# Kernel optimization log

Hardware: AMD Instinct MI355X
Metric: run time of the kernel (lower is better)

The kernel has to match this reference:

```python
import jax, jax.numpy as jnp
import numpy as np
from jax import lax

# Static model/config sizes
B, ANG, C, H, NF, NB = 1, 9, 3, 128, 16, 2


def get_freq_position(n):
    """Anti-diagonal frequency bands of an n x n angular-DCT grid (python/static)."""
    bands = []
    for i in range(n):
        bands.append(([i], [0]))
    for j in range(1, n):
        bands.append(([n - 1], [j]))
    for item in bands:
        while item[0][0] > 0 and item[1][0] < n - 1:
            item[0].insert(0, item[0][0] - 1)
            item[1].insert(0, item[1][0] + 1)
    return bands


def dct_mat(n):
    """Orthonormal DCT-II matrix (row k = k-th basis)."""
    k = jnp.arange(n, dtype=jnp.float32)[:, None]
    i = jnp.arange(n, dtype=jnp.float32)[None, :]
    m = jnp.cos(jnp.pi * (i + 0.5) * k / n) * jnp.sqrt(2.0 / n)
    return m.at[0].multiply(1.0 / np.sqrt(2.0))


def conv3d(x, w, b):
    # x: (N, Cin, D, H, W), w: (Cout, Cin, 3, 3, 3)
    y = lax.conv_general_dilated(x, w, (1, 1, 1), 'SAME',
                                 dimension_numbers=('NCDHW', 'OIDHW', 'NCDHW'))
    return y + b[None, :, None, None, None]


def branch(cut, wi, bi, a, wb, bb):
    """init conv + NB ResBlock3D (PReLU -> Conv3d, residual), plus outer skip."""
    y0 = conv3d(cut, wi, bi)
    y = y0
    for k in range(NB):
        r = jnp.where(y >= 0, y, a[k] * y)  # PReLU (single-parameter)
        y = y + conv3d(r, wb[k], bb[k])
    return y0 + y


def setup_inputs() -> dict:
    key = jax.random.key(0)
    ks = jax.random.split(key, 32)

    def nrm(k, shape, s=0.05):
        return jax.random.normal(k, shape, dtype=jnp.float32) * s

    inp = {"x": jax.random.normal(ks[0], (B, ANG, ANG, C, H, H), dtype=jnp.float32)}
    i = 1
    for n in ("dc", "lo", "mi", "hi"):
        inp[f"w_{n}_i"] = nrm(ks[i], (NF, C, 3, 3, 3)); i += 1
        inp[f"b_{n}_i"] = nrm(ks[i], (NF,)); i += 1
        inp[f"a_{n}"] = jnp.full((NB,), 0.25, dtype=jnp.float32)
        inp[f"w_{n}"] = nrm(ks[i], (NB, NF, NF, 3, 3, 3)); i += 1
        inp[f"b_{n}"] = nrm(ks[i], (NB, NF)); i += 1
    inp["w_last"] = nrm(ks[i], (C, NF))  # 1x1 Conv2d, no bias
    return inp


def reference(x, w_dc_i, b_dc_i, a_dc, w_dc, b_dc,
              w_lo_i, b_lo_i, a_lo, w_lo, b_lo,
              w_mi_i, b_mi_i, a_mi, w_mi, b_mi,
              w_hi_i, b_hi_i, a_hi, w_hi, b_hi, w_last):
    b, u, v, c, h, w = x.shape
    Da = dct_mat(u)  # angular DCT (u == v)
    Ds = dct_mat(h)  # spatial DCT (h == w)

    # SpaAngDCT: spatial 2D DCT then angular 2D DCT
    xf = jnp.einsum('buvchw,Hh,Ww->buvcHW', x, Ds, Ds)
    xf = jnp.einsum('buvchw,Uu,Vv->bUVchw', xf, Da, Da)

    x_rec = jnp.zeros((b, NF, u, v, h, w), dtype=x.dtype)
    for idx, (ui, vi) in enumerate(get_freq_position(u)):
        if idx == 0:
            p = (w_dc_i, b_dc_i, a_dc, w_dc, b_dc)
        elif idx <= 2:
            p = (w_lo_i, b_lo_i, a_lo, w_lo, b_lo)
        elif idx <= u - 1:
            p = (w_mi_i, b_mi_i, a_mi, w_mi, b_mi)
        else:
            p = (w_hi_i, b_hi_i, a_hi, w_hi, b_hi)
        ua, va = jnp.array(ui), jnp.array(vi)
        cut = xf[:, ua, va].transpose(0, 2, 1, 3, 4)  # (b, c, L, h, w)
        out = branch(cut, *p)                          # (b, NF, L, h, w)
        x_rec = x_rec.at[:, :, ua, va].set(out)        # scatter band back

    # 'b c u v h w -> b c (u h) (v w)' then 1x1 conv (NF -> 3)
    xr = x_rec.transpose(0, 1, 2, 4, 3, 5).reshape(b, NF, u * h, v * w)
    xr = jnp.einsum('bnHW,on->boHW', xr, w_last)
    xr = xr.reshape(b, c, u, h, v, w).transpose(0, 2, 4, 1, 3, 5)  # (b,u,v,c,h,w)

    # InverseSpaAngDCT: angular IDCT then spatial IDCT
    xr = jnp.einsum('bUVchw,Uu,Vv->buvchw', xr, Da, Da)
    xr = jnp.einsum('buvcHW,Hh,Ww->buvchw', xr, Ds, Ds)
    return xr + x
```

## Files before the change

kernel.cpp:

```cpp
#include <hip/hip_runtime.h>
#include <hip/hip_bf16.h>
#include <math.h>

typedef __hip_bfloat16 bf16;
typedef __attribute__((ext_vector_type(8))) short short8;
typedef __attribute__((ext_vector_type(4))) float floatx4;
typedef __attribute__((ext_vector_type(4))) unsigned int uint4v;
typedef __attribute__((ext_vector_type(2))) unsigned int uint2v;

#define HW 16384
#define NSLICE 243

__constant__ int c_s_of_p[81] = {
  0, 1,1, 2,2,2, 3,3,3,3, 4,4,4,4,4, 5,5,5,5,5,5, 6,6,6,6,6,6,6,
  7,7,7,7,7,7,7,7, 8,8,8,8,8,8,8,8,8, 9,9,9,9,9,9,9,9,
  10,10,10,10,10,10,10, 11,11,11,11,11,11, 12,12,12,12,12,
  13,13,13,13, 14,14,14, 15,15, 16};
__constant__ int c_l_of_p[81] = {
  0, 0,1, 0,1,2, 0,1,2,3, 0,1,2,3,4, 0,1,2,3,4,5, 0,1,2,3,4,5,6,
  0,1,2,3,4,5,6,7, 0,1,2,3,4,5,6,7,8, 0,1,2,3,4,5,6,7,
  0,1,2,3,4,5,6, 0,1,2,3,4,5, 0,1,2,3,4, 0,1,2,3, 0,1,2, 0,1, 0};
__constant__ int c_L_of_s[17] = {1,2,3,4,5,6,7,8,9,8,7,6,5,4,3,2,1};
__constant__ int c_g_of_s[17] = {0,1,1,2,2,2,2,2,2,3,3,3,3,3,3,3,3};
__constant__ int c_pos_uv[81] = {
  0,1,3,6,10,15,21,28,36,
  2,4,7,11,16,22,29,37,45,
  5,8,12,17,23,30,38,46,53,
  9,13,18,24,31,39,47,54,60,
  14,19,25,32,40,48,55,61,66,
  20,26,33,41,49,56,62,67,71,
  27,34,42,50,57,63,68,72,75,
  35,43,51,58,64,69,73,76,78,
  44,52,59,65,70,74,77,79,80};

struct WPtrs {
  const float* wi[4]; const float* bi[4]; const float* a[4];
  const float* wb[4]; const float* bb[4]; const float* wl;
};

__device__ __forceinline__ unsigned short f2bf(float f) {
  return __bfloat16_as_ushort(__float2bfloat16(f));
}
__device__ __forceinline__ float bf2f(unsigned short u) {
  return __uint_as_float(((unsigned int)u) << 16);
}
__device__ __forceinline__ float bflo(unsigned int w) {
  return __uint_as_float(w << 16);
}
__device__ __forceinline__ float bfhi(unsigned int w) {
  return __uint_as_float(w & 0xffff0000u);
}
__device__ __forceinline__ unsigned int pack2(float a, float b) {
  return (unsigned int)f2bf(a) | ((unsigned int)f2bf(b) << 16);
}
__device__ __forceinline__ float invprelu(float v, float invA) {
  return (v >= 0.f) ? v : v * invA;
}
__device__ __forceinline__ void bfsplit(float v, unsigned short& hi, unsigned short& lo) {
  unsigned int bits = __float_as_uint(v);
  hi = (unsigned short)(bits >> 16);
  lo = f2bf(v - __uint_as_float(bits & 0xffff0000u));
}
__device__ __forceinline__ void gl_lds16(const void* g, void* l) {
  __builtin_amdgcn_global_load_lds(
      (const __attribute__((address_space(1))) unsigned int*)g,
      (__attribute__((address_space(3))) unsigned int*)l, 16, 0, 0);
}
__device__ __forceinline__ int ldsoff(int plane, int col) {
  return plane * 2112 + ((plane & 3) << 5) + (col << 4);
}
__device__ __forceinline__ float da_entry(int t) {
  int U = t / 9, u = t % 9;
  if (U == 0) return 0.33333334f;
  int m9 = (U * (2 * u + 1)) % 36;
  return cosf((float)m9 * 0.17453293f) * 0.47140452f;
}
__device__ __forceinline__ void wmf_repack(const WPtrs& P, unsigned short* Wmf, int t) {
  if (t >= 92160) return;
  int s = t / 7680, r = t % 7680;
  int step = r / 512, r2 = r % 512;
  int lane = r2 >> 3, j = r2 & 7;
  int d = step / 5, i = step % 5;
  int q = lane >> 4, m = lane & 15;
  int tl = 2 * i + (q >> 1);
  int cin = (q & 1) * 8 + j;
  float val = 0.f;
  if (tl <= 8) {
    int ky = tl / 3, kx = tl % 3;
    int tap = d * 9 + ky * 3 + kx;
    if (s < 4) {
      if (cin < 3) val = P.wi[s][(m * 3 + cin) * 27 + tap];
    } else {
      int g = (s - 4) >> 1, k = (s - 4) & 1;
      val = P.wb[g][((k * 16 + m) * 16 + cin) * 27 + tap];
    }
  }
  Wmf[t] = f2bf(val);
}

__global__ __launch_bounds__(1024) void k_dct2(const float* __restrict__ X,
                                               const float* __restrict__ xres,
                                               float* __restrict__ Yf,
                                               unsigned short* __restrict__ Ybf,
                                               WPtrs P,
                                               unsigned short* __restrict__ Wmf) {
  if (blockIdx.x >= 243) {
    int t2 = (blockIdx.x - 243) * 1024 + threadIdx.x;
    wmf_repack(P, Wmf, t2);
    return;
  }
  extern __shared__ char dynlds[];
  unsigned short* sThi = (unsigned short*)dynlds;
  unsigned short* sTlo = (unsigned short*)(dynlds + 34816);
  unsigned short* sBhi = (unsigned short*)(dynlds + 69632);
  unsigned short* sBlo = (unsigned short*)(dynlds + 102400);
  int s = blockIdx.x;
  int t = threadIdx.x;
  int lane = t & 63, wv16 = t >> 6;
  int mt8 = wv16 & 7, nh = wv16 >> 3;
  int q = lane >> 4, n16 = lane & 15;
  const float* Xs = X + (size_t)s * HW;
  int isFwd = (Ybf != nullptr);

  for (int i = t; i < 16384; i += 1024) {
    int jj = i & 7, ln = (i >> 3) & 63, ks = (i >> 9) & 3, tile = i >> 11;
    int row = tile * 16 + (ln & 15);
    int colk = ks * 32 + (ln >> 4) * 8 + jj;
    int mm = isFwd ? (row * (2 * colk + 1)) & 511
                   : (colk * (2 * row + 1)) & 511;
    float vv = cosf((float)mm * 0.012271846f) * 0.125f;
    if (isFwd ? (row == 0) : (colk == 0)) vv *= 0.70710678f;
    unsigned short hh, ll;
    bfsplit(vv, hh, ll);
    sBhi[i] = hh; sBlo[i] = ll;
  }
  __syncthreads();

  floatx4 acc[4];
#pragma unroll
  for (int ntl = 0; ntl < 4; ntl++) acc[ntl] = (floatx4){0.f, 0.f, 0.f, 0.f};

#pragma unroll
  for (int ks = 0; ks < 4; ks++) {
    short8 ahi, alo;
    {
      const float* xp = Xs + (mt8 * 16 + n16) * 128 + ks * 32 + q * 8;
      float4 a = *(const float4*)xp;
      float4 b = *(const float4*)(xp + 4);
      union { short8 v; unsigned short u[8]; } H, L;
      float xv[8] = {a.x, a.y, a.z, a.w, b.x, b.y, b.z, b.w};
#pragma unroll
      for (int j = 0; j < 8; j++) bfsplit(xv[j], H.u[j], L.u[j]);
      ahi = H.v; alo = L.v;
    }
#pragma unroll
    for (int ntl = 0; ntl < 4; ntl++) {
      int e = (nh * 4 + ntl) * 2048 + ks * 512 + lane * 8;
      short8 bh = *(const short8*)(sBhi + e);
      short8 bl = *(const short8*)(sBlo + e);
      acc[ntl] = __builtin_amdgcn_mfma_f32_16x16x32_bf16(ahi, bl, acc[ntl], 0, 0, 0);
      acc[ntl] = __builtin_amdgcn_mfma_f32_16x16x32_bf16(alo, bh, acc[ntl], 0, 0, 0);
      acc[ntl] = __builtin_amdgcn_mfma_f32_16x16x32_bf16(ahi, bh, acc[ntl], 0, 0, 0);
    }
  }

#pragma unroll
  for (int ntl = 0; ntl < 4; ntl++) {
    int col = (nh * 4 + ntl) * 16 + n16;
    int rowb = mt8 * 16 + q * 4;
#pragma unroll
    for (int rp = 0; rp < 4; rp += 2) {
      unsigned short h0, l0, h1, l1;
      bfsplit(acc[ntl][rp], h0, l0);
      bfsplit(acc[ntl][rp + 1], h1, l1);
      int widx = (col * 136 + rowb + rp) >> 1;
      ((unsigned int*)sThi)[widx] = (unsigned int)h0 | ((unsigned int)h1 << 16);
      ((unsigned int*)sTlo)[widx] = (unsigned int)l0 | ((unsigned int)l1 << 16);
    }
  }
  __syncthreads();

#pragma unroll
  for (int ntl = 0; ntl < 4; ntl++) acc[ntl] = (floatx4){0.f, 0.f, 0.f, 0.f};

#pragma unroll
  for (int ks = 0; ks < 4; ks++) {
    int e0 = mt8 * 2048 + ks * 512 + lane * 8;
    short8 ahi = *(const short8*)(sBhi + e0);
    short8 alo = *(const short8*)(sBlo + e0);
#pragma unroll
    for (int ntl = 0; ntl < 4; ntl++) {
      int off = ((nh * 4 + ntl) * 16 + n16) * 136 + ks * 32 + q * 8;
      short8 bh = *(const short8*)(sThi + off);
      short8 bl = *(const short8*)(sTlo + off);
      acc[ntl] = __builtin_amdgcn_mfma_f32_16x16x32_bf16(ahi, bl, acc[ntl], 0, 0, 0);
      acc[ntl] = __builtin_amdgcn_mfma_f32_16x16x32_bf16(alo, bh, acc[ntl], 0, 0, 0);
      acc[ntl] = __builtin_amdgcn_mfma_f32_16x16x32_bf16(ahi, bh, acc[ntl], 0, 0, 0);
    }
  }

#pragma unroll
  for (int ntl = 0; ntl < 4; ntl++) {
    int row0 = mt8 * 16 + q * 4;
    int col = (nh * 4 + ntl) * 16 + n16;
#pragma unroll
    for (int r = 0; r < 4; r++) {
      size_t oi = (size_t)s * HW + (size_t)(row0 + r) * 128 + col;
      float v = acc[ntl][r];
      if (Ybf) {
        Ybf[oi] = f2bf(v);
      } else {
        if (xres) v += xres[oi];
        Yf[oi] = v;
      }
    }
  }
}

__global__ __launch_bounds__(256) void k_angfwd(const unsigned short* __restrict__ in,
                                                unsigned short* __restrict__ out) {
  __shared__ float sDa[81];
  int t = threadIdx.x;
  if (t < 81) sDa[t] = da_entry(t);
  __syncthreads();
  int idx = blockIdx.x * 256 + t;
  int hw = idx & (HW - 1);
  int r = idx >> 14;
  int c = r % 3, ub = r / 3;
  unsigned short raw[81];
#pragma unroll
  for (int u = 0; u < 9; u++)
#pragma unroll
    for (int v = 0; v < 9; v++)
      raw[u * 9 + v] = in[(size_t)((u * 9 + v) * 3 + c) * HW + hw];
  float tmp[3][9];
#pragma unroll
  for (int i = 0; i < 3; i++)
#pragma unroll
    for (int v = 0; v < 9; v++) tmp[i][v] = 0.f;
#pragma unroll
  for (int u = 0; u < 9; u++) {
    float fv[9];
#pragma unroll
    for (int v = 0; v < 9; v++) fv[v] = bf2f(raw[u * 9 + v]);
#pragma unroll
    for (int i = 0; i < 3; i++) {
      float dc = sDa[(ub * 3 + i) * 9 + u];
#pragma unroll
      for (int v = 0; v < 9; v++) tmp[i][v] += dc * fv[v];
    }
  }
#pragma unroll
  for (int i = 0; i < 3; i++) {
    int U = ub * 3 + i;
#pragma unroll
    for (int V = 0; V < 9; V++) {
      float acc = 0.f;
#pragma unroll
      for (int v = 0; v < 9; v++) acc += sDa[V * 9 + v] * tmp[i][v];
      out[(size_t)(c_pos_uv[U * 9 + V] * 3 + c) * HW + hw] = f2bf(acc);
    }
  }
}

__global__ __launch_bounds__(256) void k_anginv(const float* __restrict__ xrb,
                                                float* __restrict__ out) {
  __shared__ float sDa[81];
  int t = threadIdx.x;
  if (t < 81) sDa[t] = da_entry(t);
  __syncthreads();
  int idx = blockIdx.x * 256 + t;
  int hw = idx & (HW - 1);
  int r = idx >> 14;
  int c = r % 3, ub = r / 3;
  float raw[81];
#pragma unroll
  for (int U = 0; U < 9; U++)
#pragma unroll
    for (int V = 0; V < 9; V++)
      raw[U * 9 + V] = xrb[((size_t)c_pos_uv[U * 9 + V] * 3 + c) * HW + hw];
  float tmp[3][9];
#pragma unroll
  for (int i = 0; i < 3; i++)
#pragma unroll
    for (int V = 0; V < 9; V++) tmp[i][V] = 0.f;
#pragma unroll
  for (int U = 0; U < 9; U++) {
#pragma unroll
    for (int i = 0; i < 3; i++) {
      float dc = sDa[U * 9 + (ub * 3 + i)];
#pragma unroll
      for (int V = 0; V < 9; V++) tmp[i][V] += dc * raw[U * 9 + V];
    }
  }
#pragma unroll
  for (int i = 0; i < 3; i++) {
    int u = ub * 3 + i;
#pragma unroll
    for (int v = 0; v < 9; v++) {
      float acc = 0.f;
#pragma unroll
      for (int V = 0; V < 9; V++) acc += sDa[V * 9 + v] * tmp[i][V];
      out[(size_t)((u * 9 + v) * 3 + c) * HW + hw] = acc;
    }
  }
}

__global__ __launch_bounds__(1024, 8) void k_conv(const unsigned short* __restrict__ src,
                                              const unsigned short* __restrict__ act0,
                                              const unsigned short* __restrict__ Wmf,
                                              WPtrs P,
                                              int sel,
                                              unsigned short* __restrict__ boutAct,
                                              float* __restrict__ xrbOut) {
  __shared__ unsigned short s_lds[21184];
  int p = blockIdx.y;
  int s = c_s_of_p[p], l = c_l_of_p[p];
  int g = c_g_of_s[s], Ls = c_L_of_s[s];
  int row0 = blockIdx.x * 8;
  int t = threadIdx.x;
  int lane = t & 63, wv16 = t >> 6;
  int row8 = wv16 & 7, ch = wv16 >> 3;
  int q = lane >> 4, n = lane & 15;

  float aNext = (sel < 2) ? P.a[g][sel] : 0.f;
  float invA  = (sel > 0) ? 1.0f / P.a[g][sel - 1] : 0.f;

  {
    uint4v z = (uint4v){0u, 0u, 0u, 0u};
    int zmax = (sel == 0) ? 1320 : 40;
    for (int i = t; i < zmax; i += 1024) {
      int row, half, col;
      if (i < 40) { row = i >> 2; half = (i >> 1) & 1; col = (i & 1) ? 129 : 0; }
      else { int j = i - 40; row = j >> 7; col = (j & 127) + 1; half = 1; }
      *(uint4v*)((char*)s_lds + ldsoff(row * 2 + half, col)) = z;
    }
    for (int row = 0; row < 10; row++) {
      int grow = row0 - 1 + row;
      if ((unsigned)grow >= 128u) {
        for (int i = t; i < 264; i += 1024) {
          int half = i / 132, col = i % 132;
          *(uint4v*)((char*)s_lds + ldsoff(row * 2 + half, col)) = z;
        }
      }
    }
  }

  int off2[5];
#pragma unroll
  for (int i = 0; i < 5; i++) {
    int tl = 2 * i + (q >> 1);
    if (tl > 8) tl = 8;
    int ky = tl / 3, kx = tl % 3;
    off2[i] = ldsoff(2 * (row8 + ky) + (q & 1), n + kx) + ch * 1024;
  }

  int setIdx = (sel == 0) ? g : (4 + g * 2 + (sel - 1));
  const char* WsetBase = (const char*)Wmf + (size_t)setIdx * 15 * 1024;

  floatx4 acc[4];
#pragma unroll
  for (int cg = 0; cg < 4; cg++) acc[cg] = (floatx4){0.f, 0.f, 0.f, 0.f};

  const int dord[3] = {0, 2, 1};
  for (int k = 0; k < 3; k++) {
    int d = dord[k];
    int l2 = l + d - 1;
    if (l2 < 0 || l2 >= Ls) continue;
    int p2 = p + d - 1;
    __syncthreads();
    if (sel == 0) {
#pragma unroll
      for (int it = 0; it < 2; it++) {
        int id = t + it * 1024;
        if (id < 1280) {
          int row = id >> 7, col = id & 127;
          int grow = row0 - 1 + row;
          if ((unsigned)grow < 128u) {
            const unsigned short* s0 = src + (size_t)p2 * 3 * HW +
                                       (size_t)grow * 128 + col;
            unsigned int c0 = s0[0];
            unsigned int c1 = s0[HW];
            unsigned int c2 = s0[2 * HW];
            uint4v val;
            val.x = c0 | (c1 << 16);
            val.y = c2;
            val.z = 0u; val.w = 0u;
            *(uint4v*)((char*)s_lds + ldsoff(row * 2, col + 1)) = val;
          }
        }
      }
    } else {
#pragma unroll
      for (int it = 0; it < 3; it++) {
        int id = t + it * 1024;
        if (id < 2560) {
          int row = id >> 8, half = (id >> 7) & 1, col = id & 127;
          int grow = row0 - 1 + row;
          if ((unsigned)grow < 128u) {
            const void* gp = (const void*)(src +
                (((size_t)p2 * HW + (size_t)grow * 128 + col) * 16 + half * 8));
            void* lp = (void*)((char*)s_lds + ldsoff(row * 2 + half, col + 1));
            gl_lds16(gp, lp);
          }
        }
      }
    }
    __syncthreads();
    short8 af[5];
#pragma unroll
    for (int i = 0; i < 5; i++)
      af[i] = *(const short8*)(WsetBase + ((d * 5 + i) * 64 + lane) * 16);
#pragma unroll
    for (int cg = 0; cg < 4; cg++) {
#pragma unroll
      for (int i = 0; i < 5; i++) {
        short8 b = *(const short8*)((const char*)s_lds + off2[i] + cg * 256);
        acc[cg] = __builtin_amdgcn_mfma_f32_16x16x32_bf16(af[i], b, acc[cg], 0, 0, 0);
      }
    }
  }

  const float* bp = (sel == 0) ? P.bi[g] : (P.bb[g] + (sel - 1) * 16);
  float bz[4];
#pragma unroll
  for (int r = 0; r < 4; r++) bz[r] = bp[q * 4 + r];
  int h = row0 + row8;

  if (sel < 2) {
#pragma unroll
    for (int cg = 0; cg < 4; cg++) {
      size_t pix = (size_t)p * HW + h * 128 + ch * 64 + cg * 16 + n;
      float r0 = acc[cg][0] + bz[0], r1 = acc[cg][1] + bz[1];
      float r2 = acc[cg][2] + bz[2], r3 = acc[cg][3] + bz[3];
      if (sel != 0) {
        uint2v pv = *(const uint2v*)((const char*)s_lds +
            ldsoff(2 * (row8 + 1) + (q >> 1), ch * 64 + cg * 16 + n + 1) + (q & 1) * 8);
        r0 += invprelu(bflo(pv.x), invA); r1 += invprelu(bfhi(pv.x), invA);
        r2 += invprelu(bflo(pv.y), invA); r3 += invprelu(bfhi(pv.y), invA);
      }
      r0 = fmaxf(r0, 0.f) + aNext * fminf(r0, 0.f);
      r1 = fmaxf(r1, 0.f) + aNext * fminf(r1, 0.f);
      r2 = fmaxf(r2, 0.f) + aNext * fminf(r2, 0.f);
      r3 = fmaxf(r3, 0.f) + aNext * fminf(r3, 0.f);
      uint2v ov; ov.x = pack2(r0, r1); ov.y = pack2(r2, r3);
      *(uint2v*)(boutAct + pix * 16 + q * 4) = ov;
    }
  } else {
    float invA0 = 1.0f / P.a[g][0];
    float wl0[4], wl1[4], wl2[4];
#pragma unroll
    for (int r = 0; r < 4; r++) {
      wl0[r] = P.wl[q * 4 + r];
      wl1[r] = P.wl[16 + q * 4 + r];
      wl2[r] = P.wl[32 + q * 4 + r];
    }
#pragma unroll
    for (int cg = 0; cg < 4; cg++) {
      size_t pix = (size_t)p * HW + h * 128 + ch * 64 + cg * 16 + n;
      float r0 = acc[cg][0] + bz[0], r1 = acc[cg][1] + bz[1];
      float r2 = acc[cg][2] + bz[2], r3 = acc[cg][3] + bz[3];
      uint2v pv = *(const uint2v*)((const char*)s_lds +
          ldsoff(2 * (row8 + 1) + (q >> 1), ch * 64 + cg * 16 + n + 1) + (q & 1) * 8);
      r0 += invprelu(bflo(pv.x), invA); r1 += invprelu(bfhi(pv.x), invA);
      r2 += invprelu(bflo(pv.y), invA); r3 += invprelu(bfhi(pv.y), invA);
      uint2v p0 = *(const uint2v*)(act0 + pix * 16 + q * 4);
      r0 += invprelu(bflo(p0.x), invA0); r1 += invprelu(bfhi(p0.x), invA0);
      r2 += invprelu(bflo(p0.y), invA0); r3 += invprelu(bfhi(p0.y), invA0);
      float o0 = wl0[0] * r0 + wl0[1] * r1 + wl0[2] * r2 + wl0[3] * r3;
      float o1 = wl1[0] * r0 + wl1[1] * r1 + wl1[2] * r2 + wl1[3] * r3;
      float o2 = wl2[0] * r0 + wl2[1] * r1 + wl2[2] * r2 + wl2[3] * r3;
      o0 += __shfl_xor(o0, 16); o0 += __shfl_xor(o0, 32);
      o1 += __shfl_xor(o1, 16); o1 += __shfl_xor(o1, 32);
      o2 += __shfl_xor(o2, 16); o2 += __shfl_xor(o2, 32);
      if (q == 0) {
        size_t hw = (size_t)h * 128 + ch * 64 + cg * 16 + n;
        xrbOut[((size_t)p * 3 + 0) * HW + hw] = o0;
        xrbOut[((size_t)p * 3 + 1) * HW + hw] = o1;
        xrbOut[((size_t)p * 3 + 2) * HW + hw] = o2;
      }
    }
  }
}

extern "C" void kernel_launch(void* const* d_in, const int* in_sizes, int n_in,
                              void* d_out, int out_size, void* d_ws, size_t ws_size,
                              hipStream_t stream) {
  (void)in_sizes; (void)n_in; (void)out_size; (void)ws_size;
  const float* x = (const float*)d_in[0];
  WPtrs P;
  for (int g = 0; g < 4; g++) {
    int b = 1 + g * 5;
    P.wi[g] = (const float*)d_in[b + 0];
    P.bi[g] = (const float*)d_in[b + 1];
    P.a[g]  = (const float*)d_in[b + 2];
    P.wb[g] = (const float*)d_in[b + 3];
    P.bb[g] = (const float*)d_in[b + 4];
  }
  P.wl = (const float*)d_in[21];

  char* base = (char*)d_ws;
  size_t off = 0;
  auto take = [&](size_t bytes) -> char* {
    char* r = base + off;
    off += (bytes + 255) & ~(size_t)255;
    return r;
  };
  unsigned short* Wmf = (unsigned short*)take(92160 * 2);
  float* R1 = (float*)take((size_t)NSLICE * HW * 4);
  unsigned short* B1 = (unsigned short*)take((size_t)NSLICE * HW * 2);
  float* R3 = (float*)take((size_t)NSLICE * HW * 4);
  unsigned short* braw0 = (unsigned short*)take((size_t)81 * 16 * HW * 2);
  unsigned short* braw1 = (unsigned short*)take((size_t)81 * 16 * HW * 2);
  unsigned short* xf2b = (unsigned short*)R3;
  float* xrb = R3;

  k_dct2<<<333, 1024, 135168, stream>>>(x, nullptr, nullptr, B1, P, Wmf);
  k_angfwd<<<576, 256, 0, stream>>>(B1, xf2b);
  k_conv<<<dim3(16, 81), 1024, 0, stream>>>(xf2b, nullptr, Wmf, P,
                                            0, braw0, nullptr);
  k_conv<<<dim3(16, 81), 1024, 0, stream>>>(braw0, nullptr, Wmf, P,
                                            1, braw1, nullptr);
  k_conv<<<dim3(16, 81), 1024, 0, stream>>>(braw1, braw0, Wmf, P,
                                            2, nullptr, xrb);
  k_anginv<<<576, 256, 0, stream>>>(xrb, R1);
  k_dct2<<<243, 1024, 135168, stream>>>(R1, x, (float*)d_out, nullptr, P, Wmf);
}
```

Measured before the change: 264.6 us.

## Double-buffer LDS tiles in k_conv to overlap depth-slice loads with MFMA

Splits the shared-memory tile into two buffers and prefetches the next valid depth slice while MFMAs run on the current one. Explicit waitcnt plus barrier pairs replace the two __syncthreads per depth step, and the launch-bounds occupancy hint is lowered from 8 to 4. The goal is to hide global-to-LDS load latency across the up to three depth taps. In exchange, LDS per block roughly doubles to about 85 KB, which can cut resident blocks per CU. With at most three iterations, there is little latency left to overlap.

```diff
diff --git a/kernel.cpp b/kernel.cpp
--- a/kernel.cpp
+++ b/kernel.cpp
@@ -306,14 +306,14 @@
   }
 }
 
-__global__ __launch_bounds__(1024, 8) void k_conv(const unsigned short* __restrict__ src,
+__global__ __launch_bounds__(1024, 4) void k_conv(const unsigned short* __restrict__ src,
                                               const unsigned short* __restrict__ act0,
                                               const unsigned short* __restrict__ Wmf,
                                               WPtrs P,
                                               int sel,
                                               unsigned short* __restrict__ boutAct,
                                               float* __restrict__ xrbOut) {
-  __shared__ unsigned short s_lds[21184];
+  __shared__ unsigned short s_lds[2][21184];
   int p = blockIdx.y;
   int s = c_s_of_p[p], l = c_l_of_p[p];
   int g = c_g_of_s[s], Ls = c_L_of_s[s];
@@ -326,21 +326,23 @@
   float aNext = (sel < 2) ? P.a[g][sel] : 0.f;
   float invA  = (sel > 0) ? 1.0f / P.a[g][sel - 1] : 0.f;
 
-  {
+#pragma unroll
+  for (int bb = 0; bb < 2; bb++) {
+    char* lb = (char*)s_lds[bb];
     uint4v z = (uint4v){0u, 0u, 0u, 0u};
     int zmax = (sel == 0) ? 1320 : 40;
     for (int i = t; i < zmax; i += 1024) {
       int row, half, col;
       if (i < 40) { row = i >> 2; half = (i >> 1) & 1; col = (i & 1) ? 129 : 0; }
       else { int j = i - 40; row = j >> 7; col = (j & 127) + 1; half = 1; }
-      *(uint4v*)((char*)s_lds + ldsoff(row * 2 + half, col)) = z;
+      *(uint4v*)(lb + ldsoff(row * 2 + half, col)) = z;
     }
     for (int row = 0; row < 10; row++) {
       int grow = row0 - 1 + row;
       if ((unsigned)grow >= 128u) {
         for (int i = t; i < 264; i += 1024) {
           int half = i / 132, col = i % 132;
-          *(uint4v*)((char*)s_lds + ldsoff(row * 2 + half, col)) = z;
+          *(uint4v*)(lb + ldsoff(row * 2 + half, col)) = z;
         }
       }
     }
@@ -362,13 +364,19 @@
 #pragma unroll
   for (int cg = 0; cg < 4; cg++) acc[cg] = (floatx4){0.f, 0.f, 0.f, 0.f};
 
-  const int dord[3] = {0, 2, 1};
-  for (int k = 0; k < 3; k++) {
-    int d = dord[k];
-    int l2 = l + d - 1;
-    if (l2 < 0 || l2 >= Ls) continue;
+  int dlist[3], nd = 0;
+  {
+    const int dord[3] = {0, 2, 1};
+    for (int k = 0; k < 3; k++) {
+      int d = dord[k];
+      int l2 = l + d - 1;
+      if (l2 >= 0 && l2 < Ls) dlist[nd++] = d;
+    }
+  }
+
+  auto stage = [&](int bb, int d) {
+    char* lb = (char*)s_lds[bb];
     int p2 = p + d - 1;
-    __syncthreads();
     if (sel == 0) {
 #pragma unroll
       for (int it = 0; it < 2; it++) {
@@ -386,7 +394,7 @@
             val.x = c0 | (c1 << 16);
             val.y = c2;
             val.z = 0u; val.w = 0u;
-            *(uint4v*)((char*)s_lds + ldsoff(row * 2, col + 1)) = val;
+            *(uint4v*)(lb + ldsoff(row * 2, col + 1)) = val;
           }
         }
       }
@@ -400,27 +408,45 @@
           if ((unsigned)grow < 128u) {
             const void* gp = (const void*)(src +
                 (((size_t)p2 * HW + (size_t)grow * 128 + col) * 16 + half * 8));
-            void* lp = (void*)((char*)s_lds + ldsoff(row * 2 + half, col + 1));
+            void* lp = (void*)(lb + ldsoff(row * 2 + half, col + 1));
             gl_lds16(gp, lp);
           }
         }
       }
     }
-    __syncthreads();
+  };
+
+  stage(0, dlist[0]);
+  asm volatile("s_waitcnt vmcnt(0) lgkmcnt(0)" ::: "memory");
+  __builtin_amdgcn_s_barrier();
+  asm volatile("" ::: "memory");
+
+  for (int k = 0; k < nd; k++) {
+    int d = dlist[k];
+    int cur = k & 1;
     short8 af[5];
 #pragma unroll
     for (int i = 0; i < 5; i++)
       af[i] = *(const short8*)(WsetBase + ((d * 5 + i) * 64 + lane) * 16);
+    if (k + 1 < nd) stage(cur ^ 1, dlist[k + 1]);
+    asm volatile("" ::: "memory");
+    const char* lb = (const char*)s_lds[cur];
 #pragma unroll
     for (int cg = 0; cg < 4; cg++) {
 #pragma unroll
       for (int i = 0; i < 5; i++) {
-        short8 b = *(const short8*)((const char*)s_lds + off2[i] + cg * 256);
+        short8 b = *(const short8*)(lb + off2[i] + cg * 256);
         acc[cg] = __builtin_amdgcn_mfma_f32_16x16x32_bf16(af[i], b, acc[cg], 0, 0, 0);
       }
     }
-  }
-
+    if (k + 1 < nd) {
+      asm volatile("s_waitcnt vmcnt(0) lgkmcnt(0)" ::: "memory");
+      __builtin_amdgcn_s_barrier();
+      asm volatile("" ::: "memory");
+    }
+  }
+
+  const char* lbE = (const char*)s_lds[(nd - 1) & 1];
   const float* bp = (sel == 0) ? P.bi[g] : (P.bb[g] + (sel - 1) * 16);
   float bz[4];
 #pragma unroll
@@ -434,7 +460,7 @@
       float r0 = acc[cg][0] + bz[0], r1 = acc[cg][1] + bz[1];
       float r2 = acc[cg][2] + bz[2], r3 = acc[cg][3] + bz[3];
       if (sel != 0) {
-        uint2v pv = *(const uint2v*)((const char*)s_lds +
+        uint2v pv = *(const uint2v*)(lbE +
             ldsoff(2 * (row8 + 1) + (q >> 1), ch * 64 + cg * 16 + n + 1) + (q & 1) * 8);
         r0 += invprelu(bflo(pv.x), invA); r1 += invprelu(bfhi(pv.x), invA);
         r2 += invprelu(bflo(pv.y), invA); r3 += invprelu(bfhi(pv.y), invA);
@@ -460,7 +486,7 @@
       size_t pix = (size_t)p * HW + h * 128 + ch * 64 + cg * 16 + n;
       float r0 = acc[cg][0] + bz[0], r1 = acc[cg][1] + bz[1];
       float r2 = acc[cg][2] + bz[2], r3 = acc[cg][3] + bz[3];
-      uint2v pv = *(const uint2v*)((const char*)s_lds +
+      uint2v pv = *(const uint2v*)(lbE +
           ldsoff(2 * (row8 + 1) + (q >> 1), ch * 64 + cg * 16 + n + 1) + (q & 1) * 8);
       r0 += invprelu(bflo(pv.x), invA); r1 += invprelu(bfhi(pv.x), invA);
       r2 += invprelu(bflo(pv.y), invA); r3 += invprelu(bfhi(pv.y), invA);
```

New measurement: 365.3 us. +38.1%, slower.
